# Kernel tuning notes

Measured on AMD Instinct MI355X. Metric: run time of the kernel, lower is better.

The kernel has to match this reference:

```python
import jax, jax.numpy as jnp
import numpy as np
import math

N = 20000          # nodes
E = 320000         # edges (avg degree 16)
NS, NV = 16, 4     # scalar / vector multiplicities
NCAT = 10
CAT_VOCAB = 119
DIST_DIM = 32
LIG_MAX_R = 5.0
W1_NUMEL = NS * NS + NS * NV          # 320 : layer1 tp weights
W2_NUMEL = NS * NS + NV * NS + NS * NV + NV * NV + NV * NV  # 416


def setup_inputs() -> dict:
    key = jax.random.key(0)
    ks = jax.random.split(key, 24)
    s = 0.1
    inp = {
        'x_cat': jax.random.randint(ks[0], (N, NCAT), 0, 2),
        'x_scalar': jax.random.normal(ks[1], (N, 32), jnp.float32),
        'pos': jax.random.normal(ks[2], (N, 3), jnp.float32) * 3.0,
        'edge_index': jax.random.randint(ks[3], (2, E), 0, N),
        'edge_bond': jax.random.uniform(ks[4], (E, 10), jnp.float32),
        # AtomEncoder params
        'emb_tables': jax.random.normal(ks[5], (NCAT, CAT_VOCAB, NS)) * s,
        'node_w': jax.random.normal(ks[6], (32, NS)) * s,
        'node_b': jnp.zeros((NS,), jnp.float32),
        # lig_edge_embedding MLP (42 -> ns -> ns)
        'em_w1': jax.random.normal(ks[7], (10 + DIST_DIM, NS)) * s,
        'em_b1': jnp.zeros((NS,), jnp.float32),
        'em_w2': jax.random.normal(ks[8], (NS, NS)) * s,
        'em_b2': jnp.zeros((NS,), jnp.float32),
        'c1_w1': jax.random.normal(ks[9], (3 * NS, 3 * NS)) * s,
        'c1_b1': jnp.zeros((3 * NS,), jnp.float32),
        'c1_w2': jax.random.normal(ks[10], (3 * NS, W1_NUMEL)) * s,
        'c1_b2': jnp.zeros((W1_NUMEL,), jnp.float32),
        # conv layer 2 fc
        'c2_w1': jax.random.normal(ks[11], (3 * NS, 3 * NS)) * s,
        'c2_b1': jnp.zeros((3 * NS,), jnp.float32),
        'c2_w2': jax.random.normal(ks[12], (3 * NS, W2_NUMEL)) * s,
        'c2_b2': jnp.zeros((W2_NUMEL,), jnp.float32),
    }
    return inp


def _scatter_mean(vals, idx, n):
    s = jax.ops.segment_sum(vals, idx, num_segments=n)
    cnt = jax.ops.segment_sum(jnp.ones(idx.shape, vals.dtype), idx, num_segments=n)
    return s / jnp.maximum(cnt, 1.0)[:, None]


def _forward(x_cat, x_scalar, pos, edge_index, edge_bond,
             emb_tables, node_w, node_b, em_w1, em_b1, em_w2, em_b2,
             c1_w1, c1_b1, c1_w2, c1_b2, c2_w1, c2_b1, c2_w2, c2_b2):
    ns, nv = NS, NV
    n = x_cat.shape[0]
    # ---- AtomEncoder: sum of categorical embeddings + linear(scalar) ----
    gathered = emb_tables[jnp.arange(NCAT)[None, :], x_cat]      # [N, 10, ns]
    node = gathered.sum(axis=1) + x_scalar @ node_w + node_b    # [N, ns]

    src, dst = edge_index[0], edge_index[1]
    vec = pos[dst] - pos[src]                                   # [E, 3]
    dist = jnp.sqrt(jnp.sum(vec * vec, axis=-1) + 1e-12)
    unit = vec / (dist + 1e-8)[:, None]
    # spherical harmonics, lmax=1, component normalization: [1, sqrt(3)*r_hat]
    sh0 = jnp.ones((vec.shape[0], 1), vec.dtype)
    sh1 = math.sqrt(3.0) * unit                                 # [E, 3]

    # ---- GaussianSmearing + edge embedding MLP ----
    offset = jnp.linspace(0.0, LIG_MAX_R, DIST_DIM)
    coeff = -0.5 / float(LIG_MAX_R / (DIST_DIM - 1)) ** 2
    demb = jnp.exp(coeff * (dist[:, None] - offset[None, :]) ** 2)
    e_in = jnp.concatenate([edge_bond, demb], axis=1)           # [E, 42]
    edge_emb = jax.nn.relu(e_in @ em_w1 + em_b1) @ em_w2 + em_b2  # [E, ns]

    # ======== conv layer 1: ns x0e -> ns x0e + nv x1o ========
    ea = jnp.concatenate([edge_emb, node[src, :ns], node[dst, :ns]], axis=1)
    w = jax.nn.relu(ea @ c1_w1 + c1_b1) @ c1_w2 + c1_b2         # [E, 320]
    wa = w[:, :ns * ns].reshape(-1, ns, ns)
    wb = w[:, ns * ns:].reshape(-1, ns, nv)
    s_dst = node[dst]                                           # [E, ns]
    a = 1.0 / math.sqrt(ns)                                     # fan-in norm
    out0 = jnp.einsum('euk,eu->ek', wa, s_dst) * sh0 * a        # 0e x 0e -> 0e
    out1 = jnp.einsum('euw,eu->ew', wb, s_dst)[:, :, None] * sh1[:, None, :] * a
    tp = jnp.concatenate([out0, out1.reshape(-1, 3 * nv)], axis=1)
    node = _scatter_mean(tp, src, n)                            # [N, ns+3nv]

    # ======== conv layer 2: ns x0e + nv x1o -> ns x0e + nv x1o + nv x1e ====
    ea = jnp.concatenate([edge_emb, node[src, :ns], node[dst, :ns]], axis=1)
    w = jax.nn.relu(ea @ c2_w1 + c2_b1) @ c2_w2 + c2_b2         # [E, 416]
    o = 0
    wa = w[:, o:o + ns * ns].reshape(-1, ns, ns); o += ns * ns
    wb = w[:, o:o + nv * ns].reshape(-1, nv, ns); o += nv * ns
    wc = w[:, o:o + ns * nv].reshape(-1, ns, nv); o += ns * nv
    wd = w[:, o:o + nv * nv].reshape(-1, nv, nv); o += nv * nv
    we = w[:, o:o + nv * nv].reshape(-1, nv, nv)
    s = node[dst, :ns]
    v = node[dst, ns:].reshape(-1, nv, 3)
    a0 = 1.0 / math.sqrt(ns + nv)   # two paths into 0e
    a1 = 1.0 / math.sqrt(ns + nv)   # two paths into 1o
    aE = 1.0 / math.sqrt(nv)        # one path into 1e
    vdot = jnp.einsum('evi,ei->ev', v, sh1)                     # 1o . 1o
    out0 = (jnp.einsum('euk,eu->ek', wa, s) * sh0
            + jnp.einsum('euk,eu->ek', wb, vdot) / math.sqrt(3.0)) * a0
    out1o = (jnp.einsum('euw,eu->ew', wc, s)[:, :, None] * sh1[:, None, :]
             + jnp.einsum('euw,eui->ewi', wd, v) * sh0[:, :, None]) * a1
    crossv = jnp.cross(v, jnp.broadcast_to(sh1[:, None, :], v.shape))
    out1e = jnp.einsum('euw,eui->ewi', we, crossv) * (aE / math.sqrt(2.0))
    tp = jnp.concatenate([out0, out1o.reshape(-1, 3 * nv),
                          out1e.reshape(-1, 3 * nv)], axis=1)
    node = _scatter_mean(tp, src, n)                            # [N, ns+6nv] = [N,40]
    return node


def reference(x_cat, x_scalar, pos, edge_index, edge_bond,
              emb_tables, node_w, node_b, em_w1, em_b1, em_w2, em_b2,
              c1_w1, c1_b1, c1_w2, c1_b2, c2_w1, c2_b1, c2_w2, c2_b2):
    return _forward(x_cat, x_scalar, pos, edge_index, edge_bond,
                    emb_tables, node_w, node_b, em_w1, em_b1, em_w2, em_b2,
                    c1_w1, c1_b1, c1_w2, c1_b2, c2_w1, c2_b1, c2_w2, c2_b2)
```

## Files before the change

### kernel.cpp

```cpp
#include <hip/hip_runtime.h>
#include <math.h>

#define NN 20000
#define NE 320000

typedef _Float16 f16x8 __attribute__((ext_vector_type(8)));
typedef float f32x4 __attribute__((ext_vector_type(4)));
typedef unsigned short ushort_t;
typedef unsigned int uint_t;

#define MFMA16(A,B,C) __builtin_amdgcn_mfma_f32_16x16x32_f16((A),(B),(C),0,0,0)
#define LDS_FENCE() do{ asm volatile("s_waitcnt lgkmcnt(0)" ::: "memory"); __builtin_amdgcn_sched_barrier(0);}while(0)

static_assert(NE % 256 == 0, "edge grid must tile exactly");

__device__ __forceinline__ float frelu(float x){ return fmaxf(x, 0.0f); }

__device__ __forceinline__ void splitf(float x, ushort_t& h, ushort_t& l){
    _Float16 hh = (_Float16)x;
    float r = (x - (float)hh) * 2048.0f;
    _Float16 ll = (_Float16)r;
    union { _Float16 f; ushort_t u; } ch, cl;
    ch.f = hh; cl.f = ll;
    h = ch.u; l = cl.u;
}

__device__ __forceinline__ void edge_embed(
    int e, int s, int d,
    const float* __restrict__ pos,
    const float* __restrict__ edge_bond,
    const float* __restrict__ em_w1, const float* __restrict__ em_b1,
    const float* __restrict__ em_w2, const float* __restrict__ em_b2,
    float* eemb, float* sh1)
{
    float vx = pos[d*3+0] - pos[s*3+0];
    float vy = pos[d*3+1] - pos[s*3+1];
    float vz = pos[d*3+2] - pos[s*3+2];
    float d2 = vx*vx + vy*vy + vz*vz + 1e-12f;
    float dist = sqrtf(d2);
    float inv = 1.0f / (dist + 1e-8f);
    const float SQ3 = 1.7320508075688772f;
    sh1[0] = SQ3 * vx * inv;
    sh1[1] = SQ3 * vy * inv;
    sh1[2] = SQ3 * vz * inv;

    float ein[42];
    #pragma unroll
    for (int t = 0; t < 10; ++t) ein[t] = edge_bond[e*10 + t];
    const float coeff = -19.22f;
    const float step  = 5.0f / 31.0f;
    #pragma unroll
    for (int k = 0; k < 32; ++k) {
        float dd = dist - step * (float)k;
        ein[10+k] = __expf(coeff * dd * dd);
    }

    float t1[16];
    #pragma unroll
    for (int j = 0; j < 16; ++j) t1[j] = em_b1[j];
    #pragma unroll
    for (int t = 0; t < 42; ++t) {
        float v = ein[t];
        #pragma unroll
        for (int j = 0; j < 16; ++j) t1[j] += v * em_w1[t*16 + j];
    }
    #pragma unroll
    for (int j = 0; j < 16; ++j) t1[j] = frelu(t1[j]);

    #pragma unroll
    for (int j = 0; j < 16; ++j) eemb[j] = em_b2[j];
    #pragma unroll
    for (int t = 0; t < 16; ++t) {
        float v = t1[t];
        #pragma unroll
        for (int j = 0; j < 16; ++j) eemb[j] += v * em_w2[t*16 + j];
    }
}

template<int STRIDE>
__device__ __forceinline__ void compute_h(
    int e, int s, int d,
    const float* __restrict__ pos, const float* __restrict__ edge_bond,
    const float* __restrict__ em_w1, const float* __restrict__ em_b1,
    const float* __restrict__ em_w2, const float* __restrict__ em_b2,
    const float* __restrict__ w1, const float* __restrict__ b1,
    const float* __restrict__ node, float* h, float* sh1, float* sdout)
{
    float ea[48];
    edge_embed(e, s, d, pos, edge_bond, em_w1, em_b1, em_w2, em_b2, ea, sh1);
    const float4* rs = reinterpret_cast<const float4*>(node + (size_t)s*STRIDE);
    const float4* rd = reinterpret_cast<const float4*>(node + (size_t)d*STRIDE);
    #pragma unroll
    for (int k = 0; k < 4; ++k) {
        float4 q = rs[k];
        ea[16+4*k] = q.x; ea[17+4*k] = q.y; ea[18+4*k] = q.z; ea[19+4*k] = q.w;
        float4 r = rd[k];
        ea[32+4*k] = r.x; ea[33+4*k] = r.y; ea[34+4*k] = r.z; ea[35+4*k] = r.w;
    }
    #pragma unroll
    for (int k = 0; k < 16; ++k) sdout[k] = ea[32+k];
    #pragma unroll
    for (int j = 0; j < 48; ++j) h[j] = b1[j];
    #pragma unroll
    for (int t = 0; t < 48; ++t) {
        float v = ea[t];
        #pragma unroll
        for (int j = 0; j < 48; ++j) h[j] += v * w1[t*48 + j];
    }
    #pragma unroll
    for (int j = 0; j < 48; ++j) h[j] = frelu(h[j]);
}

__global__ __launch_bounds__(256)
void k_pack(const float* __restrict__ w2, const float* __restrict__ b2,
            ushort_t* __restrict__ out, int NC, int ntiles)
{
    int slot = blockIdx.x*256 + threadIdx.x;
    if (slot >= ntiles*128) return;
    int tl = slot >> 7; int r7 = slot & 127; int kb = r7 >> 6; int ll = r7 & 63;
    int col = tl*16 + (ll & 15);
    int k0 = (kb<<5) + ((ll>>4)<<3);
    uint_t hw[4], lw[4];
    #pragma unroll
    for (int p = 0; p < 4; ++p) {
        int ka = k0 + 2*p, kb2 = k0 + 2*p + 1;
        float va = (ka < 48) ? w2[ka*NC + col] : (ka == 48 ? b2[col] : 0.0f);
        float vb = (kb2 < 48) ? w2[kb2*NC + col] : (kb2 == 48 ? b2[col] : 0.0f);
        ushort_t ah, al, bh, bl;
        splitf(va, ah, al);
        splitf(vb, bh, bl);
        hw[p] = (uint_t)ah | ((uint_t)bh << 16);
        lw[p] = (uint_t)al | ((uint_t)bl << 16);
    }
    int base = tl*2048 + kb*1024 + ll*8;
    *reinterpret_cast<uint4*>(&out[base])       = make_uint4(hw[0], hw[1], hw[2], hw[3]);
    *reinterpret_cast<uint4*>(&out[base + 512]) = make_uint4(lw[0], lw[1], lw[2], lw[3]);
}

__device__ __forceinline__ void copy_chunk(ushort_t* sB, const ushort_t* __restrict__ g,
                                           int c0, int ntl, int tid)
{
    const uint4* gp = reinterpret_cast<const uint4*>(g) + c0*256;
    uint4* sp = reinterpret_cast<uint4*>(sB);
    for (int i = tid; i < ntl*256; i += 256) sp[i] = gp[i];
}

__device__ __forceinline__ void stage_A(ushort_t* bounce, int l,
                                        const uint_t* hph, const uint_t* hpl,
                                        f16x8 ahi[4][2], f16x8 alo[4][2])
{
    #pragma unroll
    for (int t = 0; t < 4; ++t)
        *reinterpret_cast<uint4*>(&bounce[l*32 + t*8]) = make_uint4(0,0,0,0);
    LDS_FENCE();
    #pragma unroll
    for (int mt = 0; mt < 4; ++mt) {
        if ((l >> 4) == mt) {
            #pragma unroll
            for (int jj = 0; jj < 25; ++jj) {
                int k = jj*2, kb = k >> 5, kk = k & 31;
                int lr = (l & 15) + ((kk >> 3) << 4);
                int off = kb*512 + lr*8 + (kk & 7);
                *reinterpret_cast<uint_t*>(&bounce[off])        = hph[jj];
                *reinterpret_cast<uint_t*>(&bounce[1024 + off]) = hpl[jj];
            }
        }
        LDS_FENCE();
        ahi[mt][0] = *reinterpret_cast<const f16x8*>(&bounce[l*8]);
        ahi[mt][1] = *reinterpret_cast<const f16x8*>(&bounce[512 + l*8]);
        alo[mt][0] = *reinterpret_cast<const f16x8*>(&bounce[1024 + l*8]);
        alo[mt][1] = *reinterpret_cast<const f16x8*>(&bounce[1536 + l*8]);
        LDS_FENCE();
    }
}

__global__ __launch_bounds__(256)
void k_node_feat(const int* __restrict__ x_cat, const float* __restrict__ x_scalar,
                 const float* __restrict__ emb, const float* __restrict__ node_w,
                 const float* __restrict__ node_b, float* __restrict__ node0)
{
    int n = blockIdx.x * 256 + threadIdx.x;
    if (n >= NN) return;
    float acc[16];
    #pragma unroll
    for (int k = 0; k < 16; ++k) acc[k] = node_b[k];
    #pragma unroll
    for (int c = 0; c < 10; ++c) {
        int idx = x_cat[n*10 + c];
        const float4* row = reinterpret_cast<const float4*>(emb + (c*119 + idx)*16);
        #pragma unroll
        for (int k = 0; k < 4; ++k) {
            float4 q = row[k];
            acc[4*k+0] += q.x; acc[4*k+1] += q.y; acc[4*k+2] += q.z; acc[4*k+3] += q.w;
        }
    }
    #pragma unroll
    for (int t = 0; t < 32; ++t) {
        float xs = x_scalar[n*32 + t];
        #pragma unroll
        for (int k = 0; k < 16; ++k) acc[k] += xs * node_w[t*16 + k];
    }
    #pragma unroll
    for (int k = 0; k < 16; ++k) node0[n*16 + k] = acc[k];
}

__global__ __launch_bounds__(256)
void k_edge_l1(const int* __restrict__ ei, const float* __restrict__ pos,
               const float* __restrict__ edge_bond,
               const float* __restrict__ em_w1, const float* __restrict__ em_b1,
               const float* __restrict__ em_w2, const float* __restrict__ em_b2,
               const float* __restrict__ w1, const float* __restrict__ b1,
               const ushort_t* __restrict__ packW,
               const float* __restrict__ node0,
               float* __restrict__ accum, float* __restrict__ cnt)
{
    __shared__ __align__(16) ushort_t sB[7*2048];
    __shared__ __align__(16) float    sT[16*260];
    __shared__ float sSh[256*3];
    __shared__ int   sSrc[256];

    int tid = threadIdx.x;
    int l = tid & 63;
    int cc = l & 15;
    int e = blockIdx.x*256 + tid;
    int s = ei[e], d = ei[NE + e];

    float h[48], sh1[3], sd[16];
    compute_h<16>(e, s, d, pos, edge_bond, em_w1, em_b1, em_w2, em_b2, w1, b1,
                  node0, h, sh1, sd);
    atomicAdd(cnt + s, 1.0f);
    sSrc[tid] = s;
    #pragma unroll
    for (int u = 0; u < 16; ++u) sT[u*260 + tid] = sd[u];
    #pragma unroll
    for (int k = 0; k < 3; ++k) sSh[tid*3 + k] = sh1[k];

    uint_t hph[25], hpl[25];
    #pragma unroll
    for (int jj = 0; jj < 24; ++jj) {
        ushort_t ah, al, bh, bl;
        splitf(h[2*jj],   ah, al);
        splitf(h[2*jj+1], bh, bl);
        hph[jj] = (uint_t)ah | ((uint_t)bh << 16);
        hpl[jj] = (uint_t)al | ((uint_t)bl << 16);
    }
    hph[24] = 0x3C00u;
    hpl[24] = 0u;

    f16x8 ahi[4][2], alo[4][2];
    stage_A(sB + (tid >> 6)*2048, l, hph, hpl, ahi, alo);

    f32x4 out0[4];
    float ob[4][4];
    #pragma unroll
    for (int mt = 0; mt < 4; ++mt) {
        out0[mt] = (f32x4){0.f,0.f,0.f,0.f};
        #pragma unroll
        for (int r = 0; r < 4; ++r) ob[mt][r] = 0.f;
    }

    for (int c0 = 0; c0 < 20; c0 += 7) {
        int ntl = (20 - c0 < 7) ? (20 - c0) : 7;
        __syncthreads();
        copy_chunk(sB, packW, c0, ntl, tid);
        __syncthreads();
        for (int tl = 0; tl < ntl; ++tl) {
            int t = c0 + tl;
            int bb = tl*2048 + l*8;
            f16x8 bh0 = *reinterpret_cast<const f16x8*>(&sB[bb]);
            f16x8 bl0 = *reinterpret_cast<const f16x8*>(&sB[bb + 512]);
            f16x8 bh1 = *reinterpret_cast<const f16x8*>(&sB[bb + 1024]);
            f16x8 bl1 = *reinterpret_cast<const f16x8*>(&sB[bb + 1536]);
            #pragma unroll
            for (int mt = 0; mt < 4; ++mt) {
                f32x4 Dh = (f32x4){0.f,0.f,0.f,0.f};
                f32x4 Dc = (f32x4){0.f,0.f,0.f,0.f};
                Dh = MFMA16(ahi[mt][0], bh0, Dh);
                Dh = MFMA16(ahi[mt][1], bh1, Dh);
                Dc = MFMA16(alo[mt][0], bh0, Dc);
                Dc = MFMA16(ahi[mt][0], bl0, Dc);
                Dc = MFMA16(alo[mt][1], bh1, Dc);
                Dc = MFMA16(ahi[mt][1], bl1, Dc);
                f32x4 D = Dh + Dc * 0.00048828125f;
                int elb = (tid & 192) + (mt << 4) + ((l >> 4) << 2);
                if (t < 16) {
                    f32x4 sv = *reinterpret_cast<const f32x4*>(&sT[t*260 + elb]);
                    out0[mt] += sv * D;
                } else {
                    const float* sp = &sT[(((t-16)<<2) + (cc>>2))*260 + elb];
                    #pragma unroll
                    for (int r = 0; r < 4; ++r) ob[mt][r] += sp[r] * D[r];
                }
            }
        }
    }

    #pragma unroll
    for (int mt = 0; mt < 4; ++mt) {
        int elb = (tid & 192) + (mt << 4) + ((l >> 4) << 2);
        #pragma unroll
        for (int r = 0; r < 4; ++r) {
            int el = elb + r;
            int sidx = sSrc[el];
            atomicAdd(accum + (size_t)sidx*28 + cc, out0[mt][r] * 0.25f);
            float x = ob[mt][r];
            x += __shfl_xor(x, 4); x += __shfl_xor(x, 8);
            int q = cc / 3; int i = cc - q*3;
            float xq = __shfl(x, (l & 48) | q);
            if (cc < 12)
                atomicAdd(accum + (size_t)sidx*28 + 16 + cc, 0.25f * xq * sSh[el*3 + i]);
        }
    }
}

__global__ __launch_bounds__(256)
void k_edge_l2(const int* __restrict__ ei, const float* __restrict__ pos,
               const float* __restrict__ edge_bond,
               const float* __restrict__ em_w1, const float* __restrict__ em_b1,
               const float* __restrict__ em_w2, const float* __restrict__ em_b2,
               const float* __restrict__ w1, const float* __restrict__ b1,
               const ushort_t* __restrict__ packW,
               const float* __restrict__ node1,
               float* __restrict__ accum2)
{
    __shared__ __align__(16) ushort_t sB[6*2048];
    __shared__ __align__(16) float    sT[16*260];
    __shared__ __align__(16) float    sVd[4*260];
    __shared__ float sSh[256*3];
    __shared__ int   sSrc[256];
    __shared__ int   sDst[256];

    int tid = threadIdx.x;
    int l = tid & 63;
    int cc = l & 15;
    int e = blockIdx.x*256 + tid;
    int s = ei[e], d = ei[NE + e];

    float h[48], sh1[3], sd[16];
    compute_h<28>(e, s, d, pos, edge_bond, em_w1, em_b1, em_w2, em_b2, w1, b1,
                  node1, h, sh1, sd);
    sSrc[tid] = s;
    sDst[tid] = d;
    #pragma unroll
    for (int u = 0; u < 16; ++u) sT[u*260 + tid] = sd[u];
    #pragma unroll
    for (int k = 0; k < 3; ++k) sSh[tid*3 + k] = sh1[k];
    {
        const float4* rv = reinterpret_cast<const float4*>(node1 + (size_t)d*28 + 16);
        float4 a = rv[0], b = rv[1], c = rv[2];
        float vv[12] = {a.x,a.y,a.z,a.w, b.x,b.y,b.z,b.w, c.x,c.y,c.z,c.w};
        const float INV_SQ3 = 0.5773502691896258f;
        #pragma unroll
        for (int u = 0; u < 4; ++u)
            sVd[u*260 + tid] = (vv[u*3]*sh1[0] + vv[u*3+1]*sh1[1] + vv[u*3+2]*sh1[2]) * INV_SQ3;
    }

    uint_t hph[25], hpl[25];
    #pragma unroll
    for (int jj = 0; jj < 24; ++jj) {
        ushort_t ah, al, bh, bl;
        splitf(h[2*jj],   ah, al);
        splitf(h[2*jj+1], bh, bl);
        hph[jj] = (uint_t)ah | ((uint_t)bh << 16);
        hpl[jj] = (uint_t)al | ((uint_t)bl << 16);
    }
    hph[24] = 0x3C00u;
    hpl[24] = 0u;

    f16x8 ahi[4][2], alo[4][2];
    stage_A(sB + (tid >> 6)*2048, l, hph, hpl, ahi, alo);

    const float A0 = 0.22360679774997896f;
    const float AE = 0.3535533905932738f;

    f32x4 out0[4];
    float outc[4][4];
    #pragma unroll
    for (int mt = 0; mt < 4; ++mt) {
        out0[mt] = (f32x4){0.f,0.f,0.f,0.f};
        #pragma unroll
        for (int r = 0; r < 4; ++r) outc[mt][r] = 0.f;
    }

    for (int c0 = 0; c0 < 26; c0 += 6) {
        int ntl = (26 - c0 < 6) ? (26 - c0) : 6;
        __syncthreads();
        copy_chunk(sB, packW, c0, ntl, tid);
        __syncthreads();
        for (int tl = 0; tl < ntl; ++tl) {
            int t = c0 + tl;
            int bb = tl*2048 + l*8;
            f16x8 bh0 = *reinterpret_cast<const f16x8*>(&sB[bb]);
            f16x8 bl0 = *reinterpret_cast<const f16x8*>(&sB[bb + 512]);
            f16x8 bh1 = *reinterpret_cast<const f16x8*>(&sB[bb + 1024]);
            f16x8 bl1 = *reinterpret_cast<const f16x8*>(&sB[bb + 1536]);
            #pragma unroll
            for (int mt = 0; mt < 4; ++mt) {
                f32x4 Dh = (f32x4){0.f,0.f,0.f,0.f};
                f32x4 Dc = (f32x4){0.f,0.f,0.f,0.f};
                Dh = MFMA16(ahi[mt][0], bh0, Dh);
                Dh = MFMA16(ahi[mt][1], bh1, Dh);
                Dc = MFMA16(alo[mt][0], bh0, Dc);
                Dc = MFMA16(ahi[mt][0], bl0, Dc);
                Dc = MFMA16(alo[mt][1], bh1, Dc);
                Dc = MFMA16(ahi[mt][1], bl1, Dc);
                f32x4 D = Dh + Dc * 0.00048828125f;
                int elb = (tid & 192) + (mt << 4) + ((l >> 4) << 2);
                if (t < 16) {
                    f32x4 sv = *reinterpret_cast<const f32x4*>(&sT[t*260 + elb]);
                    out0[mt] += sv * D;
                } else if (t < 20) {
                    f32x4 vd = *reinterpret_cast<const f32x4*>(&sVd[(t-16)*260 + elb]);
                    out0[mt] += vd * D;
                } else if (t < 24) {
                    const float* sp = &sT[(((t-20)<<2) + (cc>>2))*260 + elb];
                    #pragma unroll
                    for (int r = 0; r < 4; ++r) outc[mt][r] += sp[r] * D[r];
                } else if (t == 24) {
                    #pragma unroll
                    for (int r = 0; r < 4; ++r) {
                        int el = elb + r;
                        int dv = sDst[el];
                        const float* vp = node1 + (size_t)dv*28 + 16 + (cc>>2)*3;
                        float a0 = D[r]*vp[0], a1 = D[r]*vp[1], a2 = D[r]*vp[2];
                        a0 += __shfl_xor(a0,4); a0 += __shfl_xor(a0,8);
                        a1 += __shfl_xor(a1,4); a1 += __shfl_xor(a1,8);
                        a2 += __shfl_xor(a2,4); a2 += __shfl_xor(a2,8);
                        float xc = outc[mt][r];
                        xc += __shfl_xor(xc,4); xc += __shfl_xor(xc,8);
                        int q = cc / 3; int i = cc - q*3;
                        int srcl = (l & 48) | q;
                        float g0 = __shfl(a0, srcl), g1 = __shfl(a1, srcl), g2 = __shfl(a2, srcl);
                        float oo = (i==0) ? g0 : ((i==1) ? g1 : g2);
                        float xq = __shfl(xc, srcl);
                        if (cc < 12) {
                            float sh1i = sSh[el*3 + i];
                            atomicAdd(accum2 + (size_t)sSrc[el]*40 + 16 + cc,
                                      A0 * (xq * sh1i + oo));
                        }
                    }
                } else {
                    #pragma unroll
                    for (int r = 0; r < 4; ++r) {
                        int el = elb + r;
                        int dv = sDst[el];
                        const float* vp = node1 + (size_t)dv*28 + 16 + (cc>>2)*3;
                        float vx = vp[0], vy = vp[1], vz = vp[2];
                        float sx = sSh[el*3+0], sy = sSh[el*3+1], sz = sSh[el*3+2];
                        float cx = vy*sz - vz*sy;
                        float cy = vz*sx - vx*sz;
                        float cz = vx*sy - vy*sx;
                        float a0 = D[r]*cx, a1 = D[r]*cy, a2 = D[r]*cz;
                        a0 += __shfl_xor(a0,4); a0 += __shfl_xor(a0,8);
                        a1 += __shfl_xor(a1,4); a1 += __shfl_xor(a1,8);
                        a2 += __shfl_xor(a2,4); a2 += __shfl_xor(a2,8);
                        int q = cc / 3; int i = cc - q*3;
                        int srcl = (l & 48) | q;
                        float g0 = __shfl(a0, srcl), g1 = __shfl(a1, srcl), g2 = __shfl(a2, srcl);
                        float oo = (i==0) ? g0 : ((i==1) ? g1 : g2);
                        if (cc < 12)
                            atomicAdd(accum2 + (size_t)sSrc[el]*40 + 28 + cc, AE * oo);
                    }
                }
            }
        }
    }

    #pragma unroll
    for (int mt = 0; mt < 4; ++mt) {
        int elb = (tid & 192) + (mt << 4) + ((l >> 4) << 2);
        #pragma unroll
        for (int r = 0; r < 4; ++r) {
            int el = elb + r;
            atomicAdd(accum2 + (size_t)sSrc[el]*40 + cc, out0[mt][r] * A0);
        }
    }
}

__global__ __launch_bounds__(256)
void k_div(const float* in, float* out, const float* __restrict__ cnt, int cols, int total)
{
    int i = blockIdx.x * 256 + threadIdx.x;
    if (i >= total) return;
    int n = i / cols;
    out[i] = in[i] / fmaxf(cnt[n], 1.0f);
}

extern "C" void kernel_launch(void* const* d_in, const int* in_sizes, int n_in,
                              void* d_out, int out_size, void* d_ws, size_t ws_size,
                              hipStream_t stream) {
    const int*   x_cat     = (const int*)  d_in[0];
    const float* x_scalar  = (const float*)d_in[1];
    const float* pos       = (const float*)d_in[2];
    const int*   ei        = (const int*)  d_in[3];
    const float* edge_bond = (const float*)d_in[4];
    const float* emb       = (const float*)d_in[5];
    const float* node_w    = (const float*)d_in[6];
    const float* node_b    = (const float*)d_in[7];
    const float* em_w1     = (const float*)d_in[8];
    const float* em_b1     = (const float*)d_in[9];
    const float* em_w2     = (const float*)d_in[10];
    const float* em_b2     = (const float*)d_in[11];
    const float* c1_w1     = (const float*)d_in[12];
    const float* c1_b1     = (const float*)d_in[13];
    const float* c1_w2     = (const float*)d_in[14];
    const float* c1_b2     = (const float*)d_in[15];
    const float* c2_w1     = (const float*)d_in[16];
    const float* c2_b1     = (const float*)d_in[17];
    const float* c2_w2     = (const float*)d_in[18];
    const float* c2_b2     = (const float*)d_in[19];

    float* ws     = (float*)d_ws;
    float* node0  = ws;
    float* accum1 = ws + 320000;
    float* accum2 = ws + 880000;
    float* cnt    = ws + 1680000;
    ushort_t* packA = (ushort_t*)(ws + 1700000);
    ushort_t* packB = packA + 20*2048;

    hipMemsetAsync(accum1, 0, (size_t)(560000 + 800000 + 20000) * sizeof(float), stream);

    k_pack<<<(20*128 + 255) / 256, 256, 0, stream>>>(c1_w2, c1_b2, packA, 320, 20);
    k_pack<<<(26*128 + 255) / 256, 256, 0, stream>>>(c2_w2, c2_b2, packB, 416, 26);

    k_node_feat<<<(NN + 255) / 256, 256, 0, stream>>>(
        x_cat, x_scalar, emb, node_w, node_b, node0);

    k_edge_l1<<<NE / 256, 256, 0, stream>>>(
        ei, pos, edge_bond, em_w1, em_b1, em_w2, em_b2,
        c1_w1, c1_b1, packA, node0, accum1, cnt);

    k_div<<<(560000 + 255) / 256, 256, 0, stream>>>(accum1, accum1, cnt, 28, 560000);

    k_edge_l2<<<NE / 256, 256, 0, stream>>>(
        ei, pos, edge_bond, em_w1, em_b1, em_w2, em_b2,
        c2_w1, c2_b1, packB, accum1, accum2);

    k_div<<<(800000 + 255) / 256, 256, 0, stream>>>(accum2, (float*)d_out, cnt, 40, 800000);
}
```

Measured before the change: 340.6 us.

## Load packed B weights directly from global with register prefetch instead of LDS staging

Removes the cooperative LDS staging of the packed weight tiles in both edge kernels. Each lane now loads its B fragments straight from global (L2/L1-resident) memory and prefetches the next tile into registers one iteration ahead. Shared memory is merged into a single aliased buffer reused by stage_A and the per-edge scalars, which shrinks the LDS footprint to raise occupancy and drops the per-chunk barriers. The cost is more register pressure and global/L1 traffic per wave, since every wave re-reads the weights.

```diff
diff --git a/kernel.cpp b/kernel.cpp
--- a/kernel.cpp
+++ b/kernel.cpp
@@ -137,12 +137,15 @@
     *reinterpret_cast<uint4*>(&out[base + 512]) = make_uint4(lw[0], lw[1], lw[2], lw[3]);
 }
 
-__device__ __forceinline__ void copy_chunk(ushort_t* sB, const ushort_t* __restrict__ g,
-                                           int c0, int ntl, int tid)
-{
-    const uint4* gp = reinterpret_cast<const uint4*>(g) + c0*256;
-    uint4* sp = reinterpret_cast<uint4*>(sB);
-    for (int i = tid; i < ntl*256; i += 256) sp[i] = gp[i];
+struct B4 { f16x8 h0, l0, h1, l1; };
+__device__ __forceinline__ B4 loadB(const f16x8* __restrict__ g, int t, int l) {
+    B4 b;
+    const f16x8* p = g + t*256 + l;
+    b.h0 = p[0];
+    b.l0 = p[64];
+    b.h1 = p[128];
+    b.l1 = p[192];
+    return b;
 }
 
 __device__ __forceinline__ void stage_A(ushort_t* bounce, int l,
@@ -214,10 +217,10 @@
                const float* __restrict__ node0,
                float* __restrict__ accum, float* __restrict__ cnt)
 {
-    __shared__ __align__(16) ushort_t sB[7*2048];
-    __shared__ __align__(16) float    sT[16*260];
-    __shared__ float sSh[256*3];
-    __shared__ int   sSrc[256];
+    __shared__ __align__(16) unsigned char smem[20736];
+    float* sT  = (float*)smem;
+    float* sSh = (float*)(smem + 16640);
+    int*   sSrc= (int*)(smem + 19712);
 
     int tid = threadIdx.x;
     int l = tid & 63;
@@ -229,11 +232,6 @@
     compute_h<16>(e, s, d, pos, edge_bond, em_w1, em_b1, em_w2, em_b2, w1, b1,
                   node0, h, sh1, sd);
     atomicAdd(cnt + s, 1.0f);
-    sSrc[tid] = s;
-    #pragma unroll
-    for (int u = 0; u < 16; ++u) sT[u*260 + tid] = sd[u];
-    #pragma unroll
-    for (int k = 0; k < 3; ++k) sSh[tid*3 + k] = sh1[k];
 
     uint_t hph[25], hpl[25];
     #pragma unroll
@@ -248,7 +246,15 @@
     hpl[24] = 0u;
 
     f16x8 ahi[4][2], alo[4][2];
-    stage_A(sB + (tid >> 6)*2048, l, hph, hpl, ahi, alo);
+    stage_A((ushort_t*)smem + (tid >> 6)*2048, l, hph, hpl, ahi, alo);
+
+    __syncthreads();
+    sSrc[tid] = s;
+    #pragma unroll
+    for (int u = 0; u < 16; ++u) sT[u*260 + tid] = sd[u];
+    #pragma unroll
+    for (int k = 0; k < 3; ++k) sSh[tid*3 + k] = sh1[k];
+    __syncthreads();
 
     f32x4 out0[4];
     float ob[4][4];
@@ -259,40 +265,34 @@
         for (int r = 0; r < 4; ++r) ob[mt][r] = 0.f;
     }
 
-    for (int c0 = 0; c0 < 20; c0 += 7) {
-        int ntl = (20 - c0 < 7) ? (20 - c0) : 7;
-        __syncthreads();
-        copy_chunk(sB, packW, c0, ntl, tid);
-        __syncthreads();
-        for (int tl = 0; tl < ntl; ++tl) {
-            int t = c0 + tl;
-            int bb = tl*2048 + l*8;
-            f16x8 bh0 = *reinterpret_cast<const f16x8*>(&sB[bb]);
-            f16x8 bl0 = *reinterpret_cast<const f16x8*>(&sB[bb + 512]);
-            f16x8 bh1 = *reinterpret_cast<const f16x8*>(&sB[bb + 1024]);
-            f16x8 bl1 = *reinterpret_cast<const f16x8*>(&sB[bb + 1536]);
-            #pragma unroll
-            for (int mt = 0; mt < 4; ++mt) {
-                f32x4 Dh = (f32x4){0.f,0.f,0.f,0.f};
-                f32x4 Dc = (f32x4){0.f,0.f,0.f,0.f};
-                Dh = MFMA16(ahi[mt][0], bh0, Dh);
-                Dh = MFMA16(ahi[mt][1], bh1, Dh);
-                Dc = MFMA16(alo[mt][0], bh0, Dc);
-                Dc = MFMA16(ahi[mt][0], bl0, Dc);
-                Dc = MFMA16(alo[mt][1], bh1, Dc);
-                Dc = MFMA16(ahi[mt][1], bl1, Dc);
-                f32x4 D = Dh + Dc * 0.00048828125f;
-                int elb = (tid & 192) + (mt << 4) + ((l >> 4) << 2);
-                if (t < 16) {
-                    f32x4 sv = *reinterpret_cast<const f32x4*>(&sT[t*260 + elb]);
-                    out0[mt] += sv * D;
-                } else {
-                    const float* sp = &sT[(((t-16)<<2) + (cc>>2))*260 + elb];
-                    #pragma unroll
-                    for (int r = 0; r < 4; ++r) ob[mt][r] += sp[r] * D[r];
-                }
+    const f16x8* gB = reinterpret_cast<const f16x8*>(packW);
+    B4 cur = loadB(gB, 0, l);
+    #pragma unroll 1
+    for (int t = 0; t < 20; ++t) {
+        B4 nxt;
+        if (t + 1 < 20) nxt = loadB(gB, t + 1, l);
+        #pragma unroll
+        for (int mt = 0; mt < 4; ++mt) {
+            f32x4 Dh = (f32x4){0.f,0.f,0.f,0.f};
+            f32x4 Dc = (f32x4){0.f,0.f,0.f,0.f};
+            Dh = MFMA16(ahi[mt][0], cur.h0, Dh);
+            Dh = MFMA16(ahi[mt][1], cur.h1, Dh);
+            Dc = MFMA16(alo[mt][0], cur.h0, Dc);
+            Dc = MFMA16(ahi[mt][0], cur.l0, Dc);
+            Dc = MFMA16(alo[mt][1], cur.h1, Dc);
+            Dc = MFMA16(ahi[mt][1], cur.l1, Dc);
+            f32x4 D = Dh + Dc * 0.00048828125f;
+            int elb = (tid & 192) + (mt << 4) + ((l >> 4) << 2);
+            if (t < 16) {
+                f32x4 sv = *reinterpret_cast<const f32x4*>(&sT[t*260 + elb]);
+                out0[mt] += sv * D;
+            } else {
+                const float* sp = &sT[(((t-16)<<2) + (cc>>2))*260 + elb];
+                #pragma unroll
+                for (int r = 0; r < 4; ++r) ob[mt][r] += sp[r] * D[r];
             }
         }
+        cur = nxt;
     }
 
     #pragma unroll
@@ -323,12 +323,12 @@
                const float* __restrict__ node1,
                float* __restrict__ accum2)
 {
-    __shared__ __align__(16) ushort_t sB[6*2048];
-    __shared__ __align__(16) float    sT[16*260];
-    __shared__ __align__(16) float    sVd[4*260];
-    __shared__ float sSh[256*3];
-    __shared__ int   sSrc[256];
-    __shared__ int   sDst[256];
+    __shared__ __align__(16) unsigned char smem[25920];
+    float* sT  = (float*)smem;
+    float* sVd = (float*)(smem + 16640);
+    float* sSh = (float*)(smem + 20800);
+    int*   sSrc= (int*)(smem + 23872);
+    int*   sDst= (int*)(smem + 24896);
 
     int tid = threadIdx.x;
     int l = tid & 63;
@@ -339,12 +339,8 @@
     float h[48], sh1[3], sd[16];
     compute_h<28>(e, s, d, pos, edge_bond, em_w1, em_b1, em_w2, em_b2, w1, b1,
                   node1, h, sh1, sd);
-    sSrc[tid] = s;
-    sDst[tid] = d;
-    #pragma unroll
-    for (int u = 0; u < 16; ++u) sT[u*260 + tid] = sd[u];
-    #pragma unroll
-    for (int k = 0; k < 3; ++k) sSh[tid*3 + k] = sh1[k];
+
+    float vdr[4];
     {
         const float4* rv = reinterpret_cast<const float4*>(node1 + (size_t)d*28 + 16);
         float4 a = rv[0], b = rv[1], c = rv[2];
@@ -352,7 +348,7 @@
         const float INV_SQ3 = 0.5773502691896258f;
         #pragma unroll
         for (int u = 0; u < 4; ++u)
-            sVd[u*260 + tid] = (vv[u*3]*sh1[0] + vv[u*3+1]*sh1[1] + vv[u*3+2]*sh1[2]) * INV_SQ3;
+            vdr[u] = (vv[u*3]*sh1[0] + vv[u*3+1]*sh1[1] + vv[u*3+2]*sh1[2]) * INV_SQ3;
     }
 
     uint_t hph[25], hpl[25];
@@ -368,7 +364,18 @@
     hpl[24] = 0u;
 
     f16x8 ahi[4][2], alo[4][2];
-    stage_A(sB + (tid >> 6)*2048, l, hph, hpl, ahi, alo);
+    stage_A((ushort_t*)smem + (tid >> 6)*2048, l, hph, hpl, ahi, alo);
+
+    __syncthreads();
+    sSrc[tid] = s;
+    sDst[tid] = d;
+    #pragma unroll
+    for (int u = 0; u < 16; ++u) sT[u*260 + tid] = sd[u];
+    #pragma unroll
+    for (int u = 0; u < 4; ++u) sVd[u*260 + tid] = vdr[u];
+    #pragma unroll
+    for (int k = 0; k < 3; ++k) sSh[tid*3 + k] = sh1[k];
+    __syncthreads();
 
     const float A0 = 0.22360679774997896f;
     const float AE = 0.3535533905932738f;
@@ -382,88 +389,82 @@
         for (int r = 0; r < 4; ++r) outc[mt][r] = 0.f;
     }
 
-    for (int c0 = 0; c0 < 26; c0 += 6) {
-        int ntl = (26 - c0 < 6) ? (26 - c0) : 6;
-        __syncthreads();
-        copy_chunk(sB, packW, c0, ntl, tid);
-        __syncthreads();
-        for (int tl = 0; tl < ntl; ++tl) {
-            int t = c0 + tl;
-            int bb = tl*2048 + l*8;
-            f16x8 bh0 = *reinterpret_cast<const f16x8*>(&sB[bb]);
-            f16x8 bl0 = *reinterpret_cast<const f16x8*>(&sB[bb + 512]);
-            f16x8 bh1 = *reinterpret_cast<const f16x8*>(&sB[bb + 1024]);
-            f16x8 bl1 = *reinterpret_cast<const f16x8*>(&sB[bb + 1536]);
-            #pragma unroll
-            for (int mt = 0; mt < 4; ++mt) {
-                f32x4 Dh = (f32x4){0.f,0.f,0.f,0.f};
-                f32x4 Dc = (f32x4){0.f,0.f,0.f,0.f};
-                Dh = MFMA16(ahi[mt][0], bh0, Dh);
-                Dh = MFMA16(ahi[mt][1], bh1, Dh);
-                Dc = MFMA16(alo[mt][0], bh0, Dc);
-                Dc = MFMA16(ahi[mt][0], bl0, Dc);
-                Dc = MFMA16(alo[mt][1], bh1, Dc);
-                Dc = MFMA16(ahi[mt][1], bl1, Dc);
-                f32x4 D = Dh + Dc * 0.00048828125f;
-                int elb = (tid & 192) + (mt << 4) + ((l >> 4) << 2);
-                if (t < 16) {
-                    f32x4 sv = *reinterpret_cast<const f32x4*>(&sT[t*260 + elb]);
-                    out0[mt] += sv * D;
-                } else if (t < 20) {
-                    f32x4 vd = *reinterpret_cast<const f32x4*>(&sVd[(t-16)*260 + elb]);
-                    out0[mt] += vd * D;
-                } else if (t < 24) {
-                    const float* sp = &sT[(((t-20)<<2) + (cc>>2))*260 + elb];
-                    #pragma unroll
-                    for (int r = 0; r < 4; ++r) outc[mt][r] += sp[r] * D[r];
-                } else if (t == 24) {
-                    #pragma unroll
-                    for (int r = 0; r < 4; ++r) {
-                        int el = elb + r;
-                        int dv = sDst[el];
-                        const float* vp = node1 + (size_t)dv*28 + 16 + (cc>>2)*3;
-                        float a0 = D[r]*vp[0], a1 = D[r]*vp[1], a2 = D[r]*vp[2];
-                        a0 += __shfl_xor(a0,4); a0 += __shfl_xor(a0,8);
-                        a1 += __shfl_xor(a1,4); a1 += __shfl_xor(a1,8);
-                        a2 += __shfl_xor(a2,4); a2 += __shfl_xor(a2,8);
-                        float xc = outc[mt][r];
-                        xc += __shfl_xor(xc,4); xc += __shfl_xor(xc,8);
-                        int q = cc / 3; int i = cc - q*3;
-                        int srcl = (l & 48) | q;
-                        float g0 = __shfl(a0, srcl), g1 = __shfl(a1, srcl), g2 = __shfl(a2, srcl);
-                        float oo = (i==0) ? g0 : ((i==1) ? g1 : g2);
-                        float xq = __shfl(xc, srcl);
-                        if (cc < 12) {
-                            float sh1i = sSh[el*3 + i];
-                            atomicAdd(accum2 + (size_t)sSrc[el]*40 + 16 + cc,
-                                      A0 * (xq * sh1i + oo));
-                        }
+    const f16x8* gB = reinterpret_cast<const f16x8*>(packW);
+    B4 cur = loadB(gB, 0, l);
+    #pragma unroll 1
+    for (int t = 0; t < 26; ++t) {
+        B4 nxt;
+        if (t + 1 < 26) nxt = loadB(gB, t + 1, l);
+        #pragma unroll
+        for (int mt = 0; mt < 4; ++mt) {
+            f32x4 Dh = (f32x4){0.f,0.f,0.f,0.f};
+            f32x4 Dc = (f32x4){0.f,0.f,0.f,0.f};
+            Dh = MFMA16(ahi[mt][0], cur.h0, Dh);
+            Dh = MFMA16(ahi[mt][1], cur.h1, Dh);
+            Dc = MFMA16(alo[mt][0], cur.h0, Dc);
+            Dc = MFMA16(ahi[mt][0], cur.l0, Dc);
+            Dc = MFMA16(alo[mt][1], cur.h1, Dc);
+            Dc = MFMA16(ahi[mt][1], cur.l1, Dc);
+            f32x4 D = Dh + Dc * 0.00048828125f;
+            int elb = (tid & 192) + (mt << 4) + ((l >> 4) << 2);
+            if (t < 16) {
+                f32x4 sv = *reinterpret_cast<const f32x4*>(&sT[t*260 + elb]);
+                out0[mt] += sv * D;
+            } else if (t < 20) {
+                f32x4 vd = *reinterpret_cast<const f32x4*>(&sVd[(t-16)*260 + elb]);
+                out0[mt] += vd * D;
+            } else if (t < 24) {
+                const float* sp = &sT[(((t-20)<<2) + (cc>>2))*260 + elb];
+                #pragma unroll
+                for (int r = 0; r < 4; ++r) outc[mt][r] += sp[r] * D[r];
+            } else if (t == 24) {
+                #pragma unroll
+                for (int r = 0; r < 4; ++r) {
+                    int el = elb + r;
+                    int dv = sDst[el];
+                    const float* vp = node1 + (size_t)dv*28 + 16 + (cc>>2)*3;
+                    float a0 = D[r]*vp[0], a1 = D[r]*vp[1], a2 = D[r]*vp[2];
+                    a0 += __shfl_xor(a0,4); a0 += __shfl_xor(a0,8);
+                    a1 += __shfl_xor(a1,4); a1 += __shfl_xor(a1,8);
+                    a2 += __shfl_xor(a2,4); a2 += __shfl_xor(a2,8);
+                    float xc = outc[mt][r];
+                    xc += __shfl_xor(xc,4); xc += __shfl_xor(xc,8);
+                    int q = cc / 3; int i = cc - q*3;
+                    int srcl = (l & 48) | q;
+                    float g0 = __shfl(a0, srcl), g1 = __shfl(a1, srcl), g2 = __shfl(a2, srcl);
+                    float oo = (i==0) ? g0 : ((i==1) ? g1 : g2);
+                    float xq = __shfl(xc, srcl);
+                    if (cc < 12) {
+                        float sh1i = sSh[el*3 + i];
+                        atomicAdd(accum2 + (size_t)sSrc[el]*40 + 16 + cc,
+                                  A0 * (xq * sh1i + oo));
                     }
-                } else {
-                    #pragma unroll
-                    for (int r = 0; r < 4; ++r) {
-                        int el = elb + r;
-                        int dv = sDst[el];
-                        const float* vp = node1 + (size_t)dv*28 + 16 + (cc>>2)*3;
-                        float vx = vp[0], vy = vp[1], vz = vp[2];
-                        float sx = sSh[el*3+0], sy = sSh[el*3+1], sz = sSh[el*3+2];
-                        float cx = vy*sz - vz*sy;
-                        float cy = vz*sx - vx*sz;
-                        float cz = vx*sy - vy*sx;
-                        float a0 = D[r]*cx, a1 = D[r]*cy, a2 = D[r]*cz;
-                        a0 += __shfl_xor(a0,4); a0 += __shfl_xor(a0,8);
-                        a1 += __shfl_xor(a1,4); a1 += __shfl_xor(a1,8);
-                        a2 += __shfl_xor(a2,4); a2 += __shfl_xor(a2,8);
-                        int q = cc / 3; int i = cc - q*3;
-                        int srcl = (l & 48) | q;
-                        float g0 = __shfl(a0, srcl), g1 = __shfl(a1, srcl), g2 = __shfl(a2, srcl);
-                        float oo = (i==0) ? g0 : ((i==1) ? g1 : g2);
-                        if (cc < 12)
-                            atomicAdd(accum2 + (size_t)sSrc[el]*40 + 28 + cc, AE * oo);
-                    }
+                }
+            } else {
+                #pragma unroll
+                for (int r = 0; r < 4; ++r) {
+                    int el = elb + r;
+                    int dv = sDst[el];
+                    const float* vp = node1 + (size_t)dv*28 + 16 + (cc>>2)*3;
+                    float vx = vp[0], vy = vp[1], vz = vp[2];
+                    float sx = sSh[el*3+0], sy = sSh[el*3+1], sz = sSh[el*3+2];
+                    float cx = vy*sz - vz*sy;
+                    float cy = vz*sx - vx*sz;
+                    float cz = vx*sy - vy*sx;
+                    float a0 = D[r]*cx, a1 = D[r]*cy, a2 = D[r]*cz;
+                    a0 += __shfl_xor(a0,4); a0 += __shfl_xor(a0,8);
+                    a1 += __shfl_xor(a1,4); a1 += __shfl_xor(a1,8);
+                    a2 += __shfl_xor(a2,4); a2 += __shfl_xor(a2,8);
+                    int q = cc / 3; int i = cc - q*3;
+                    int srcl = (l & 48) | q;
+                    float g0 = __shfl(a0, srcl), g1 = __shfl(a1, srcl), g2 = __shfl(a2, srcl);
+                    float oo = (i==0) ? g0 : ((i==1) ? g1 : g2);
+                    if (cc < 12)
+                        atomicAdd(accum2 + (size_t)sSrc[el]*40 + 28 + cc, AE * oo);
                 }
             }
         }
+        cur = nxt;
     }
 
     #pragma unroll
```

Result: faster. 328.6 us (-3.5%).
